# Kernel optimization log

Hardware: AMD Instinct MI355X
Metric: run time of the kernel (lower is better)

Reference implementation:

```python
import jax, jax.numpy as jnp
import numpy as np

H = 1024
S = 32768

def setup_inputs() -> dict:
    key = jax.random.key(0)
    k1, k2, k3, k4 = jax.random.split(key, 4)
    hidden = jax.random.normal(k1, (H,), dtype=jnp.float32)
    encoder_outputs = jax.random.normal(k2, (S, H), dtype=jnp.float32)
    # nn.Linear(H, H) params, scaled like torch default init
    bound = 1.0 / np.sqrt(H)
    W = jax.random.uniform(k3, (H, H), minval=-bound, maxval=bound, dtype=jnp.float32)
    b = jax.random.uniform(k4, (H,), minval=-bound, maxval=bound, dtype=jnp.float32)
    return {"hidden": hidden, "encoder_outputs": encoder_outputs, "W": W, "b": b}

def reference(hidden, encoder_outputs, W, b):
    # method == 'general': energy_i = hidden . (W @ e_i + b)
    # batched over all timesteps in one matmul instead of a Python loop
    proj = jnp.einsum('sh,dh->sd', encoder_outputs, W) + b  # [S, H]
    energies = proj @ hidden                                 # [S]
    attn = jax.nn.softmax(energies)                          # softmax over seq_len
    return attn[None, None, :]                               # [1, 1, S]
```

## Files before the change

kernel.cpp:

```cpp
#include <hip/hip_runtime.h>
#include <math.h>

#define H 1024
#define S 32768


__global__ __launch_bounds__(256) void compute_v(const float* __restrict__ W,
                                                 const float* __restrict__ hidden,
                                                 float* __restrict__ v) {
    int h = blockIdx.x * 256 + threadIdx.x;
    int d0 = blockIdx.y * 16;
    float acc = 0.f;
#pragma unroll
    for (int j = 0; j < 16; ++j) {
        int d = d0 + j;
        acc += W[(size_t)d * H + h] * hidden[d];
    }
    atomicAdd(&v[h], acc);
}

__global__ __launch_bounds__(256) void energies_kernel(const float* __restrict__ enc,
                                                       const float* __restrict__ v,
                                                       float* __restrict__ energies,
                                                       float* __restrict__ pmax,
                                                       float* __restrict__ psum) {
    const int lane = threadIdx.x & 63;
    const int wave = threadIdx.x >> 6;

    const float4* v4 = (const float4*)v;
    float4 va = v4[lane];
    float4 vb = v4[64 + lane];
    float4 vc = v4[128 + lane];
    float4 vd = v4[192 + lane];

    const int s0 = blockIdx.x * 16 + wave * 4;
    const float4* base = (const float4*)(enc + (size_t)s0 * H);

    float dot[4];
#pragma unroll
    for (int r = 0; r < 4; ++r) {
        const float4* row = base + r * (H / 4);
        float4 a = row[lane];
        float4 b = row[64 + lane];
        float4 c = row[128 + lane];
        float4 d = row[192 + lane];
        float t = a.x * va.x + a.y * va.y + a.z * va.z + a.w * va.w;
        t += b.x * vb.x + b.y * vb.y + b.z * vb.z + b.w * vb.w;
        t += c.x * vc.x + c.y * vc.y + c.z * vc.z + c.w * vc.w;
        t += d.x * vd.x + d.y * vd.y + d.z * vd.z + d.w * vd.w;
        dot[r] = t;
    }

#pragma unroll
    for (int off = 32; off > 0; off >>= 1) {
#pragma unroll
        for (int r = 0; r < 4; ++r) dot[r] += __shfl_xor(dot[r], off, 64);
    }

    if (lane == 0) {
        float4 e = make_float4(dot[0], dot[1], dot[2], dot[3]);
        *(float4*)(energies + s0) = e;
    }

    float m = fmaxf(fmaxf(dot[0], dot[1]), fmaxf(dot[2], dot[3]));
    float sum = __expf(dot[0] - m) + __expf(dot[1] - m) +
                __expf(dot[2] - m) + __expf(dot[3] - m);

    __shared__ float wm[4], wsum[4];
    if (lane == 0) { wm[wave] = m; wsum[wave] = sum; }
    __syncthreads();
    if (threadIdx.x == 0) {
        float M = wm[0], Sm = wsum[0];
#pragma unroll
        for (int w = 1; w < 4; ++w) {
            float Mn = fmaxf(M, wm[w]);
            Sm = Sm * __expf(M - Mn) + wsum[w] * __expf(wm[w] - Mn);
            M = Mn;
        }
        pmax[blockIdx.x] = M;
        psum[blockIdx.x] = Sm;
    }
}

__global__ __launch_bounds__(1024) void combine(const float* __restrict__ pmax,
                                                const float* __restrict__ psum,
                                                float* __restrict__ MS) {
    const int tid = threadIdx.x;
    const int lane = tid & 63;
    const int wave = tid >> 6;

    float m1 = pmax[tid], s1 = psum[tid];
    float m2 = pmax[tid + 1024], s2 = psum[tid + 1024];
    float M = fmaxf(m1, m2);
    float Sv = s1 * __expf(m1 - M) + s2 * __expf(m2 - M);

#pragma unroll
    for (int off = 32; off > 0; off >>= 1) {
        float Mo = __shfl_xor(M, off, 64);
        float So = __shfl_xor(Sv, off, 64);
        float Mn = fmaxf(M, Mo);
        Sv = Sv * __expf(M - Mn) + So * __expf(Mo - Mn);
        M = Mn;
    }

    __shared__ float sm[16], ss[16];
    if (lane == 0) { sm[wave] = M; ss[wave] = Sv; }
    __syncthreads();
    if (wave == 0) {
        float Mv = (lane < 16) ? sm[lane] : -INFINITY;
        float Sw = (lane < 16) ? ss[lane] : 0.f;
#pragma unroll
        for (int off = 8; off > 0; off >>= 1) {
            float Mo = __shfl_xor(Mv, off, 64);
            float So = __shfl_xor(Sw, off, 64);
            float Mn = fmaxf(Mv, Mo);
            Sw = Sw * __expf(Mv - Mn) + So * __expf(Mo - Mn);
            Mv = Mn;
        }
        if (lane == 0) {
            MS[0] = Mv;
            MS[1] = 1.0f / Sw;
        }
    }
}

__global__ __launch_bounds__(256) void finalize(float* __restrict__ out,
                                                const float* __restrict__ MS) {
    int i = blockIdx.x * 256 + threadIdx.x;
    float M = MS[0];
    float inv = MS[1];
    float4 e = ((const float4*)out)[i];
    float4 o;
    o.x = __expf(e.x - M) * inv;
    o.y = __expf(e.y - M) * inv;
    o.z = __expf(e.z - M) * inv;
    o.w = __expf(e.w - M) * inv;
    ((float4*)out)[i] = o;
}

extern "C" void kernel_launch(void* const* d_in, const int* in_sizes, int n_in,
                              void* d_out, int out_size, void* d_ws, size_t ws_size,
                              hipStream_t stream) {
    const float* hidden = (const float*)d_in[0];
    const float* enc    = (const float*)d_in[1];
    const float* W      = (const float*)d_in[2];

    float* ws   = (float*)d_ws;
    float* v    = ws;
    float* pmax = ws + 1024;
    float* psum = ws + 3072;
    float* MS   = ws + 5120;
    float* out  = (float*)d_out;

    hipMemsetAsync(v, 0, H * sizeof(float), stream);
    compute_v<<<dim3(4, 64), 256, 0, stream>>>(W, hidden, v);
    energies_kernel<<<S / 16, 256, 0, stream>>>(enc, v, out, pmax, psum);
    combine<<<1, 1024, 0, stream>>>(pmax, psum, MS);
    finalize<<<S / 4 / 256, 256, 0, stream>>>(out, MS);
}
```

Baseline: 203.5 us.

## Fold softmax combine into energies kernel via last-block counter; nontemporal loads

Removes the separate single-block combine kernel by having each energies block atomically increment a counter, with the last-arriving block reducing all partial max/sum pairs and writing the final max and reciprocal sum. The encoder-output reads also switch to nontemporal loads so the large streaming matrix does not pollute cache. This saves one kernel launch and its dependency gap, at the cost of a threadfence plus atomic per block and a serialized tail reduction in the last block.

```diff
diff --git a/kernel.cpp b/kernel.cpp
--- a/kernel.cpp
+++ b/kernel.cpp
@@ -3,6 +3,8 @@
 
 #define H 1024
 #define S 32768
+
+typedef float f4 __attribute__((ext_vector_type(4)));
 
 
 __global__ __launch_bounds__(256) void compute_v(const float* __restrict__ W,
@@ -23,27 +25,29 @@
                                                        const float* __restrict__ v,
                                                        float* __restrict__ energies,
                                                        float* __restrict__ pmax,
-                                                       float* __restrict__ psum) {
+                                                       float* __restrict__ psum,
+                                                       int* __restrict__ counter,
+                                                       float* __restrict__ MS) {
     const int lane = threadIdx.x & 63;
     const int wave = threadIdx.x >> 6;
 
-    const float4* v4 = (const float4*)v;
-    float4 va = v4[lane];
-    float4 vb = v4[64 + lane];
-    float4 vc = v4[128 + lane];
-    float4 vd = v4[192 + lane];
+    const f4* v4 = (const f4*)v;
+    f4 va = v4[lane];
+    f4 vb = v4[64 + lane];
+    f4 vc = v4[128 + lane];
+    f4 vd = v4[192 + lane];
 
     const int s0 = blockIdx.x * 16 + wave * 4;
-    const float4* base = (const float4*)(enc + (size_t)s0 * H);
+    const f4* base = (const f4*)(enc + (size_t)s0 * H);
 
     float dot[4];
 #pragma unroll
     for (int r = 0; r < 4; ++r) {
-        const float4* row = base + r * (H / 4);
-        float4 a = row[lane];
-        float4 b = row[64 + lane];
-        float4 c = row[128 + lane];
-        float4 d = row[192 + lane];
+        const f4* row = base + r * (H / 4);
+        f4 a = __builtin_nontemporal_load(row + lane);
+        f4 b = __builtin_nontemporal_load(row + 64 + lane);
+        f4 c = __builtin_nontemporal_load(row + 128 + lane);
+        f4 d = __builtin_nontemporal_load(row + 192 + lane);
         float t = a.x * va.x + a.y * va.y + a.z * va.z + a.w * va.w;
         t += b.x * vb.x + b.y * vb.y + b.z * vb.z + b.w * vb.w;
         t += c.x * vc.x + c.y * vc.y + c.z * vc.z + c.w * vc.w;
@@ -67,6 +71,7 @@
                 __expf(dot[2] - m) + __expf(dot[3] - m);
 
     __shared__ float wm[4], wsum[4];
+    __shared__ int is_last;
     if (lane == 0) { wm[wave] = m; wsum[wave] = sum; }
     __syncthreads();
     if (threadIdx.x == 0) {
@@ -79,47 +84,43 @@
         }
         pmax[blockIdx.x] = M;
         psum[blockIdx.x] = Sm;
+        __threadfence();
+        int ret = atomicAdd(counter, 1);
+        is_last = (ret == (int)gridDim.x - 1);
     }
-}
+    __syncthreads();
 
-__global__ __launch_bounds__(1024) void combine(const float* __restrict__ pmax,
-                                                const float* __restrict__ psum,
-                                                float* __restrict__ MS) {
-    const int tid = threadIdx.x;
-    const int lane = tid & 63;
-    const int wave = tid >> 6;
-
-    float m1 = pmax[tid], s1 = psum[tid];
-    float m2 = pmax[tid + 1024], s2 = psum[tid + 1024];
-    float M = fmaxf(m1, m2);
-    float Sv = s1 * __expf(m1 - M) + s2 * __expf(m2 - M);
-
+    if (is_last) {
+        __threadfence();
+        const int tid = threadIdx.x;
+        float M = -INFINITY, Sv = 0.f;
 #pragma unroll
-    for (int off = 32; off > 0; off >>= 1) {
-        float Mo = __shfl_xor(M, off, 64);
-        float So = __shfl_xor(Sv, off, 64);
-        float Mn = fmaxf(M, Mo);
-        Sv = Sv * __expf(M - Mn) + So * __expf(Mo - Mn);
-        M = Mn;
-    }
-
-    __shared__ float sm[16], ss[16];
-    if (lane == 0) { sm[wave] = M; ss[wave] = Sv; }
-    __syncthreads();
-    if (wave == 0) {
-        float Mv = (lane < 16) ? sm[lane] : -INFINITY;
-        float Sw = (lane < 16) ? ss[lane] : 0.f;
+        for (int i = tid; i < 2048; i += 256) {
+            float mi = pmax[i], si = psum[i];
+            float Mn = fmaxf(M, mi);
+            Sv = Sv * __expf(M - Mn) + si * __expf(mi - Mn);
+            M = Mn;
+        }
 #pragma unroll
-        for (int off = 8; off > 0; off >>= 1) {
-            float Mo = __shfl_xor(Mv, off, 64);
-            float So = __shfl_xor(Sw, off, 64);
-            float Mn = fmaxf(Mv, Mo);
-            Sw = Sw * __expf(Mv - Mn) + So * __expf(Mo - Mn);
-            Mv = Mn;
+        for (int off = 32; off > 0; off >>= 1) {
+            float Mo = __shfl_xor(M, off, 64);
+            float So = __shfl_xor(Sv, off, 64);
+            float Mn = fmaxf(M, Mo);
+            Sv = Sv * __expf(M - Mn) + So * __expf(Mo - Mn);
+            M = Mn;
         }
-        if (lane == 0) {
-            MS[0] = Mv;
-            MS[1] = 1.0f / Sw;
+        if (lane == 0) { wm[wave] = M; wsum[wave] = Sv; }
+        __syncthreads();
+        if (tid == 0) {
+            float Mf = wm[0], Sf = wsum[0];
+#pragma unroll
+            for (int w = 1; w < 4; ++w) {
+                float Mn = fmaxf(Mf, wm[w]);
+                Sf = Sf * __expf(Mf - Mn) + wsum[w] * __expf(wm[w] - Mn);
+                Mf = Mn;
+            }
+            MS[0] = Mf;
+            MS[1] = 1.0f / Sf;
         }
     }
 }
@@ -145,16 +146,16 @@
     const float* enc    = (const float*)d_in[1];
     const float* W      = (const float*)d_in[2];
 
-    float* ws   = (float*)d_ws;
-    float* v    = ws;
-    float* pmax = ws + 1024;
-    float* psum = ws + 3072;
-    float* MS   = ws + 5120;
-    float* out  = (float*)d_out;
+    float* ws      = (float*)d_ws;
+    float* v       = ws;
+    int*   counter = (int*)(ws + 1024);
+    float* pmax    = ws + 1028;
+    float* psum    = ws + 3076;
+    float* MS      = ws + 5124;
+    float* out     = (float*)d_out;
 
-    hipMemsetAsync(v, 0, H * sizeof(float), stream);
+    hipMemsetAsync(ws, 0, (1024 + 4) * sizeof(float), stream);
     compute_v<<<dim3(4, 64), 256, 0, stream>>>(W, hidden, v);
-    energies_kernel<<<S / 16, 256, 0, stream>>>(enc, v, out, pmax, psum);
-    combine<<<1, 1024, 0, stream>>>(pmax, psum, MS);
+    energies_kernel<<<S / 16, 256, 0, stream>>>(enc, v, out, pmax, psum, counter, MS);
     finalize<<<S / 4 / 256, 256, 0, stream>>>(out, MS);
 }
```

Result: slower. 301.8 us (+48.3%).
